# Kernel optimization log

Hardware: AMD Instinct MI355X
Metric: run time of the kernel (lower is better)

The kernel has to match this reference:

```python
import jax, jax.numpy as jnp
import numpy as np

B, H, K, D = 4096, 512, 32, 20


def setup_inputs() -> dict:
    key = jax.random.key(0)
    k1, k2 = jax.random.split(key)
    hidden = jax.random.normal(k1, (B, H), dtype=jnp.float32)
    # cluster: soft assignment probabilities (rows sum to 1), like a softmax output
    c = jax.random.uniform(k2, (B, K), dtype=jnp.float32)
    cluster = c / jnp.sum(c, axis=-1, keepdims=True)
    return {"hidden": hidden, "cluster": cluster, "d": D}


def reference(hidden, cluster, d):
    # softHidden[b,h,k] = hidden[b,h] * cluster[b,k]
    soft_hidden = hidden[:, :, None] * cluster[:, None, :]          # [B,H,K]
    class_sums = jnp.sum(soft_hidden, axis=0)                        # [H,K] (code calls these "class_means" but they are sums)
    within = jnp.sum((soft_hidden - class_sums[None]) ** 2, axis=0)  # [H,K]
    # round() has zero gradient in torch; mirror that with stop_gradient
    counts = jax.lax.stop_gradient(jnp.round(jnp.sum(cluster, axis=0)))  # [K]

    m = class_sums.T   # [K,H]
    w = within.T       # [K,H]

    # all class pairs i<j (the nested Python loops, vectorized)
    i, j = jnp.triu_indices(K, k=1)   # each [P], P = K*(K-1)/2
    mi, mj = m[i], m[j]                               # [P,H]
    gm = (mi + mj) / 2.0
    between = (mi - gm) ** 2 * counts[i][:, None] + (mj - gm) ** 2 * counts[j][:, None]
    pair_within = w[i] + w[j]                         # [P,H]
    pair_count = counts[i] + counts[j]                # [P]

    d2 = pair_count - 2.0
    d2 = jnp.where(d2 == 0.0, d2 + 1e-5, d2)
    x = between / (between + pair_within)
    x = jnp.clip(x, 1e-37, 1.0 - 1e-5)
    # regularized incomplete beta I_x(d1/2, d2/2) with d1 = 1
    xbetainc = jax.scipy.special.betainc(0.5, (d2 / 2.0)[:, None], x)  # [P,H]

    top_k, _ = jax.lax.top_k(xbetainc, d)             # [P,d]
    per_pair = jnp.sum(jnp.log(top_k), axis=-1)       # [P]
    return -jnp.sum(per_pair)
```

## Files before the change

### kernel.cpp

```cpp
#include <hip/hip_runtime.h>
#include <math.h>

#define BB 4096
#define HH 512
#define KK 32
#define PAIRS ((KK * (KK - 1)) / 2)

constexpr int TH  = 16;
constexpr int NBB = 16;
constexpr int BC  = BB / NBB;
constexpr int SUB = 64;

__global__ __launch_bounds__(256) void stage1_kernel(
    const float* __restrict__ hidden, const float* __restrict__ cluster,
    float* __restrict__ msum, float* __restrict__ s2sum,
    float* __restrict__ colsum)
{
    __shared__ float hid_s [SUB * TH];
    __shared__ float hid2_s[SUB * TH];
    __shared__ float clu_s [SUB * KK];
    __shared__ float red   [8 * TH * KK];

    const int t  = threadIdx.x;
    const int ty = t >> 5;
    const int tx = t & 31;
    const int h0 = blockIdx.x * TH;
    const int bchunk = blockIdx.y * BC;

    float acc_m[TH], acc_s[TH];
#pragma unroll
    for (int i = 0; i < TH; ++i) { acc_m[i] = 0.f; acc_s[i] = 0.f; }
    float csum = 0.f;

    const float4* hid4 = (const float4*)hidden;
    const float4* clu4 = (const float4*)cluster;

    for (int sub = 0; sub < BC; sub += SUB) {
        const int b0 = bchunk + sub;
        {
            int r = t >> 2, q = t & 3;
            float4 v = hid4[(size_t)(b0 + r) * (HH / 4) + (h0 >> 2) + q];
            ((float4*)hid_s)[t] = v;
            float4 v2; v2.x = v.x * v.x; v2.y = v.y * v.y;
            v2.z = v.z * v.z; v2.w = v.w * v.w;
            ((float4*)hid2_s)[t] = v2;
        }
#pragma unroll
        for (int e = 0; e < 2; ++e) {
            int u = t + e * 256;
            int r = u >> 3, q = u & 7;
            ((float4*)clu_s)[u] = clu4[(size_t)(b0 + r) * (KK / 4) + q];
        }
        __syncthreads();

#pragma unroll
        for (int s = 0; s < SUB / 8; ++s) {
            int r = s * 8 + ty;
            float c  = clu_s[r * KK + tx];
            float c2 = c * c;
            csum += c;
#pragma unroll
            for (int hh = 0; hh < TH; ++hh) {
                acc_m[hh] = fmaf(hid_s [r * TH + hh], c,  acc_m[hh]);
                acc_s[hh] = fmaf(hid2_s[r * TH + hh], c2, acc_s[hh]);
            }
        }
        __syncthreads();
    }

    if (blockIdx.x == 0) atomicAdd(&colsum[tx], csum);

#pragma unroll
    for (int hh = 0; hh < TH; ++hh) red[ty * (TH * KK) + hh * KK + tx] = acc_m[hh];
    __syncthreads();
    for (int u = t; u < TH * KK; u += 256) {
        float v = 0.f;
#pragma unroll
        for (int g = 0; g < 8; ++g) v += red[g * (TH * KK) + u];
        int hh = u >> 5, k = u & 31;
        atomicAdd(&msum[(size_t)k * HH + h0 + hh], v);
    }
    __syncthreads();
#pragma unroll
    for (int hh = 0; hh < TH; ++hh) red[ty * (TH * KK) + hh * KK + tx] = acc_s[hh];
    __syncthreads();
    for (int u = t; u < TH * KK; u += 256) {
        float v = 0.f;
#pragma unroll
        for (int g = 0; g < 8; ++g) v += red[g * (TH * KK) + u];
        int hh = u >> 5, k = u & 31;
        atomicAdd(&s2sum[(size_t)k * HH + h0 + hh], v);
    }
}

__device__ float betacf_dev(float a, float b, float x)
{
    const float FPMIN = 1e-30f, EPS = 1e-6f;
    float qab = a + b, qap = a + 1.0f, qam = a - 1.0f;
    float c = 1.0f;
    float d = 1.0f - qab * x / qap;
    if (fabsf(d) < FPMIN) d = FPMIN;
    d = 1.0f / d;
    float h = d;
    for (int m = 1; m <= 200; ++m) {
        float m2 = 2.0f * (float)m;
        float aa = (float)m * (b - (float)m) * x / ((qam + m2) * (a + m2));
        d = 1.0f + aa * d; if (fabsf(d) < FPMIN) d = FPMIN;
        c = 1.0f + aa / c; if (fabsf(c) < FPMIN) c = FPMIN;
        d = 1.0f / d;
        h *= d * c;
        aa = -(a + (float)m) * (qab + (float)m) * x / ((a + m2) * (qap + m2));
        d = 1.0f + aa * d; if (fabsf(d) < FPMIN) d = FPMIN;
        c = 1.0f + aa / c; if (fabsf(c) < FPMIN) c = FPMIN;
        d = 1.0f / d;
        float del = d * c;
        h *= del;
        if (fabsf(del - 1.0f) < EPS) break;
    }
    return h;
}

__global__ __launch_bounds__(256) void stage2_kernel(
    const float* __restrict__ msum, const float* __restrict__ s2sum,
    const float* __restrict__ colsum, const int* __restrict__ dptr,
    float* __restrict__ out)
{
    __shared__ float L[HH];
    __shared__ float rv[4];
    __shared__ int   ri[4];
    __shared__ float lg_s;

    const int t = threadIdx.x;
    const int p = blockIdx.x;

    int i = 0, rem = p;
    while (true) { int row = KK - 1 - i; if (rem < row) break; rem -= row; ++i; }
    const int j = i + 1 + rem;

    const float ci = roundf(colsum[i]);
    const float cj = roundf(colsum[j]);
    const float pc = ci + cj;
    float d2 = pc - 2.0f;
    if (d2 == 0.0f) d2 = 1e-5f;
    const float a = 0.5f;
    const float b = 0.5f * d2;

    if (t == 0) {
        lg_s = (float)(lgamma((double)a + (double)b)
                       - 0.57236494292470008707
                       - lgamma((double)b));
    }
    __syncthreads();
    const float lg = lg_s;
    const float xsplit = (a + 1.0f) / (a + b + 2.0f);

    for (int h = t; h < HH; h += 256) {
        float mi = msum[(size_t)i * HH + h];
        float mj = msum[(size_t)j * HH + h];
        float wi = fmaf((float)(BB - 2) * mi, mi, s2sum[(size_t)i * HH + h]);
        float wj = fmaf((float)(BB - 2) * mj, mj, s2sum[(size_t)j * HH + h]);
        float dm = 0.5f * (mi - mj);
        float between = dm * dm * pc;
        float pw = wi + wj;
        float denom = between + pw;
        float x   = between / denom;
        float omx = pw / denom;
        if (!(x >= 1e-37f)) { x = 1e-37f; omx = 1.0f; }
        if (omx < 1e-5f)    { omx = 1e-5f; x = 1.0f - 1e-5f; }

        float lbt = lg + a * logf(x) + b * logf(omx);
        float Lh;
        if (x < xsplit) {
            float cf = fmaxf(betacf_dev(a, b, x), 1e-30f);
            Lh = lbt + logf(2.0f * cf);
        } else {
            float cf = fmaxf(betacf_dev(b, a, omx), 1e-30f);
            float tt = expf(lbt) * cf / b;
            tt = fminf(tt, 0.9999999f);
            Lh = log1pf(-tt);
        }
        L[h] = Lh;
    }
    __syncthreads();

    const int d = *dptr;
    float ssum = 0.f;
    for (int r = 0; r < d; ++r) {
        float v = -INFINITY; int idx = 0;
        for (int h = t; h < HH; h += 256) {
            float lv = L[h];
            if (lv > v) { v = lv; idx = h; }
        }
#pragma unroll
        for (int off = 32; off > 0; off >>= 1) {
            float ov = __shfl_down(v, off);
            int   oi = __shfl_down(idx, off);
            if (ov > v) { v = ov; idx = oi; }
        }
        if ((t & 63) == 0) { rv[t >> 6] = v; ri[t >> 6] = idx; }
        __syncthreads();
        if (t == 0) {
            float bv = rv[0]; int bi = ri[0];
#pragma unroll
            for (int w = 1; w < 4; ++w)
                if (rv[w] > bv) { bv = rv[w]; bi = ri[w]; }
            ssum += bv;
            L[bi] = -INFINITY;
        }
        __syncthreads();
    }
    if (t == 0) atomicAdd(out, -ssum);
}

extern "C" void kernel_launch(void* const* d_in, const int* in_sizes, int n_in,
                              void* d_out, int out_size, void* d_ws, size_t ws_size,
                              hipStream_t stream)
{
    const float* hidden  = (const float*)d_in[0];
    const float* cluster = (const float*)d_in[1];
    const int*   dptr    = (const int*)d_in[2];

    float* msum   = (float*)d_ws;
    float* s2sum  = msum + HH * KK;
    float* colsum = s2sum + HH * KK;

    size_t zbytes = (size_t)(2 * HH * KK + KK) * sizeof(float);
    hipMemsetAsync(d_ws, 0, zbytes, stream);
    hipMemsetAsync(d_out, 0, sizeof(float), stream);

    dim3 g1(HH / TH, NBB);
    stage1_kernel<<<g1, 256, 0, stream>>>(hidden, cluster, msum, s2sum, colsum);
    stage2_kernel<<<PAIRS, 256, 0, stream>>>(msum, s2sum, colsum, dptr,
                                             (float*)d_out);
}
```

Baseline: 115.5 us.

## Select top-d by x before betainc and shrink stage2 to one wavefront

Stage 2 now picks the top-d x values per pair with a single 64-lane wavefront using shuffle and ballot argmax, and evaluates the continued-fraction betainc only for those d values rather than for all 512 columns. This relies on the regularized incomplete beta being monotone in x, and it removes most of the expensive continued-fraction work and the block-level synchronisation. The continued fraction also switches to hardware reciprocal approximations, a looser tolerance, a 100-iteration cap and a wave-uniform exit, and lgamma moves from double to float. Stage 1 squares hidden in registers instead of keeping a second shared array. These precision reductions may shift the result slightly.

```diff
diff --git a/kernel.cpp b/kernel.cpp
--- a/kernel.cpp
+++ b/kernel.cpp
@@ -17,7 +17,6 @@
     float* __restrict__ colsum)
 {
     __shared__ float hid_s [SUB * TH];
-    __shared__ float hid2_s[SUB * TH];
     __shared__ float clu_s [SUB * KK];
     __shared__ float red   [8 * TH * KK];
 
@@ -39,11 +38,8 @@
         const int b0 = bchunk + sub;
         {
             int r = t >> 2, q = t & 3;
-            float4 v = hid4[(size_t)(b0 + r) * (HH / 4) + (h0 >> 2) + q];
-            ((float4*)hid_s)[t] = v;
-            float4 v2; v2.x = v.x * v.x; v2.y = v.y * v.y;
-            v2.z = v.z * v.z; v2.w = v.w * v.w;
-            ((float4*)hid2_s)[t] = v2;
+            ((float4*)hid_s)[t] =
+                hid4[(size_t)(b0 + r) * (HH / 4) + (h0 >> 2) + q];
         }
 #pragma unroll
         for (int e = 0; e < 2; ++e) {
@@ -61,8 +57,9 @@
             csum += c;
 #pragma unroll
             for (int hh = 0; hh < TH; ++hh) {
-                acc_m[hh] = fmaf(hid_s [r * TH + hh], c,  acc_m[hh]);
-                acc_s[hh] = fmaf(hid2_s[r * TH + hh], c2, acc_s[hh]);
+                float hv = hid_s[r * TH + hh];
+                acc_m[hh] = fmaf(hv,      c,  acc_m[hh]);
+                acc_s[hh] = fmaf(hv * hv, c2, acc_s[hh]);
             }
         }
         __syncthreads();
@@ -93,44 +90,46 @@
     }
 }
 
-__device__ float betacf_dev(float a, float b, float x)
-{
-    const float FPMIN = 1e-30f, EPS = 1e-6f;
+__device__ __forceinline__ float frcp(float x) {
+#if __has_builtin(__builtin_amdgcn_rcpf)
+    return __builtin_amdgcn_rcpf(x);
+#else
+    return 1.0f / x;
+#endif
+}
+__device__ __forceinline__ float guardf(float t) {
+    return (fabsf(t) < 1e-30f) ? 1e-30f : t;
+}
+
+__device__ float betacf_fast(float a, float b, float x)
+{
+    const float EPS = 1e-5f;
     float qab = a + b, qap = a + 1.0f, qam = a - 1.0f;
     float c = 1.0f;
-    float d = 1.0f - qab * x / qap;
-    if (fabsf(d) < FPMIN) d = FPMIN;
-    d = 1.0f / d;
+    float d = frcp(guardf(1.0f - qab * x * frcp(qap)));
     float h = d;
-    for (int m = 1; m <= 200; ++m) {
-        float m2 = 2.0f * (float)m;
-        float aa = (float)m * (b - (float)m) * x / ((qam + m2) * (a + m2));
-        d = 1.0f + aa * d; if (fabsf(d) < FPMIN) d = FPMIN;
-        c = 1.0f + aa / c; if (fabsf(c) < FPMIN) c = FPMIN;
-        d = 1.0f / d;
+    for (int m = 1; m <= 100; ++m) {
+        float fm = (float)m, m2 = 2.0f * fm;
+        float aa = fm * (b - fm) * x * frcp((qam + m2) * (a + m2));
+        d = frcp(guardf(fmaf(aa, d, 1.0f)));
+        c = guardf(fmaf(aa, frcp(c), 1.0f));
         h *= d * c;
-        aa = -(a + (float)m) * (qab + (float)m) * x / ((a + m2) * (qap + m2));
-        d = 1.0f + aa * d; if (fabsf(d) < FPMIN) d = FPMIN;
-        c = 1.0f + aa / c; if (fabsf(c) < FPMIN) c = FPMIN;
-        d = 1.0f / d;
+        float aa2 = -(a + fm) * (qab + fm) * x * frcp((a + m2) * (qap + m2));
+        d = frcp(guardf(fmaf(aa2, d, 1.0f)));
+        c = guardf(fmaf(aa2, frcp(c), 1.0f));
         float del = d * c;
         h *= del;
-        if (fabsf(del - 1.0f) < EPS) break;
+        if (__all(fabsf(del - 1.0f) < EPS)) break;
     }
     return h;
 }
 
-__global__ __launch_bounds__(256) void stage2_kernel(
+__global__ __launch_bounds__(64) void stage2_kernel(
     const float* __restrict__ msum, const float* __restrict__ s2sum,
     const float* __restrict__ colsum, const int* __restrict__ dptr,
     float* __restrict__ out)
 {
-    __shared__ float L[HH];
-    __shared__ float rv[4];
-    __shared__ int   ri[4];
-    __shared__ float lg_s;
-
-    const int t = threadIdx.x;
+    const int lane = threadIdx.x;
     const int p = blockIdx.x;
 
     int i = 0, rem = p;
@@ -144,72 +143,77 @@
     if (d2 == 0.0f) d2 = 1e-5f;
     const float a = 0.5f;
     const float b = 0.5f * d2;
-
-    if (t == 0) {
-        lg_s = (float)(lgamma((double)a + (double)b)
-                       - 0.57236494292470008707
-                       - lgamma((double)b));
-    }
-    __syncthreads();
-    const float lg = lg_s;
+    const float lg = lgammaf(a + b) - lgammaf(b) - 0.57236494f;
     const float xsplit = (a + 1.0f) / (a + b + 2.0f);
 
-    for (int h = t; h < HH; h += 256) {
-        float mi = msum[(size_t)i * HH + h];
-        float mj = msum[(size_t)j * HH + h];
-        float wi = fmaf((float)(BB - 2) * mi, mi, s2sum[(size_t)i * HH + h]);
-        float wj = fmaf((float)(BB - 2) * mj, mj, s2sum[(size_t)j * HH + h]);
+    const float* mi_p = msum  + (size_t)i * HH;
+    const float* mj_p = msum  + (size_t)j * HH;
+    const float* si_p = s2sum + (size_t)i * HH;
+    const float* sj_p = s2sum + (size_t)j * HH;
+
+    float lv[8];
+#pragma unroll
+    for (int q = 0; q < 8; ++q) {
+        int h = q * 64 + lane;
+        float mi = mi_p[h], mj = mj_p[h];
+        float wi = fmaf((float)(BB - 2) * mi, mi, si_p[h]);
+        float wj = fmaf((float)(BB - 2) * mj, mj, sj_p[h]);
         float dm = 0.5f * (mi - mj);
         float between = dm * dm * pc;
-        float pw = wi + wj;
-        float denom = between + pw;
-        float x   = between / denom;
-        float omx = pw / denom;
-        if (!(x >= 1e-37f)) { x = 1e-37f; omx = 1.0f; }
-        if (omx < 1e-5f)    { omx = 1e-5f; x = 1.0f - 1e-5f; }
-
-        float lbt = lg + a * logf(x) + b * logf(omx);
-        float Lh;
-        if (x < xsplit) {
-            float cf = fmaxf(betacf_dev(a, b, x), 1e-30f);
-            Lh = lbt + logf(2.0f * cf);
-        } else {
-            float cf = fmaxf(betacf_dev(b, a, omx), 1e-30f);
-            float tt = expf(lbt) * cf / b;
-            tt = fminf(tt, 0.9999999f);
-            Lh = log1pf(-tt);
-        }
-        L[h] = Lh;
-    }
-    __syncthreads();
+        float denom = between + wi + wj;
+        float x = between / denom;
+        if (!(x >= 1e-37f)) x = 1e-37f;
+        x = fminf(x, 1.0f - 1e-5f);
+        lv[q] = x;
+    }
 
     const int d = *dptr;
-    float ssum = 0.f;
+
+    float myx = 0.004f;
+    float lm = lv[0];
+#pragma unroll
+    for (int q = 1; q < 8; ++q) lm = fmaxf(lm, lv[q]);
+
     for (int r = 0; r < d; ++r) {
-        float v = -INFINITY; int idx = 0;
-        for (int h = t; h < HH; h += 256) {
-            float lv = L[h];
-            if (lv > v) { v = lv; idx = h; }
-        }
-#pragma unroll
-        for (int off = 32; off > 0; off >>= 1) {
-            float ov = __shfl_down(v, off);
-            int   oi = __shfl_down(idx, off);
-            if (ov > v) { v = ov; idx = oi; }
-        }
-        if ((t & 63) == 0) { rv[t >> 6] = v; ri[t >> 6] = idx; }
-        __syncthreads();
-        if (t == 0) {
-            float bv = rv[0]; int bi = ri[0];
-#pragma unroll
-            for (int w = 1; w < 4; ++w)
-                if (rv[w] > bv) { bv = rv[w]; bi = ri[w]; }
-            ssum += bv;
-            L[bi] = -INFINITY;
-        }
-        __syncthreads();
-    }
-    if (t == 0) atomicAdd(out, -ssum);
+        float gm = lm;
+#pragma unroll
+        for (int off = 1; off < 64; off <<= 1)
+            gm = fmaxf(gm, __shfl_xor(gm, off));
+        unsigned long long msk = __ballot(lm == gm);
+        int winner = __ffsll((unsigned long long)msk) - 1;
+        if (lane == r) myx = gm;
+        if (lane == winner) {
+            bool done = false;
+#pragma unroll
+            for (int q = 0; q < 8; ++q)
+                if (!done && lv[q] == gm) { lv[q] = -1.0f; done = true; }
+            lm = lv[0];
+#pragma unroll
+            for (int q = 1; q < 8; ++q) lm = fmaxf(lm, lv[q]);
+        }
+    }
+
+    float x   = myx;
+    float omx = 1.0f - x;
+    bool  brA = x < xsplit;
+    float al  = brA ? a : b;
+    float be  = brA ? b : a;
+    float xx  = brA ? x : omx;
+    float cf  = betacf_fast(al, be, xx);
+    float lbt = lg + 0.5f * logf(x) + b * logf(omx);
+    float L;
+    if (brA) {
+        L = lbt + logf(2.0f * fmaxf(cf, 1e-30f));
+    } else {
+        float tt = expf(lbt) * cf / b;
+        tt = fminf(tt, 0.99999988f);
+        L = log1pf(-tt);
+    }
+
+    float val = (lane < d) ? L : 0.0f;
+#pragma unroll
+    for (int off = 1; off < 64; off <<= 1) val += __shfl_xor(val, off);
+    if (lane == 0) atomicAdd(out, -val);
 }
 
 extern "C" void kernel_launch(void* const* d_in, const int* in_sizes, int n_in,
@@ -230,6 +234,6 @@
 
     dim3 g1(HH / TH, NBB);
     stage1_kernel<<<g1, 256, 0, stream>>>(hidden, cluster, msum, s2sum, colsum);
-    stage2_kernel<<<PAIRS, 256, 0, stream>>>(msum, s2sum, colsum, dptr,
-                                             (float*)d_out);
-}
+    stage2_kernel<<<PAIRS, 64, 0, stream>>>(msum, s2sum, colsum, dptr,
+                                            (float*)d_out);
+}
```

Measured after the change: 102.8 us. 1.12x faster.
